# Kernel optimization log

Hardware: AMD Instinct MI355X
Metric: run time of the kernel (lower is better)

## Reference

```python
import jax, jax.numpy as jnp
import numpy as np

TAGSET = 32
START = 30
STOP = 31
B = 512
S = 2048


def setup_inputs() -> dict:
    key = jax.random.key(0)
    k1, k2, k3 = jax.random.split(key, 3)
    emissions = jax.random.normal(k1, (B, S, TAGSET), dtype=jnp.float32)
    transitions = jax.random.normal(k2, (TAGSET, TAGSET), dtype=jnp.float32)
    # replicate the torch init: no transition into START, none out of STOP
    transitions = transitions.at[START, :].set(-10000.0).at[:, STOP].set(-10000.0)
    tags = jax.random.randint(k3, (B, S), 0, START)  # valid label tags only
    return {"emissions": emissions, "transitions": transitions, "tags": tags}


def _partition(emissions, transitions):
    # CRF forward algorithm (log partition), vectorized scan over time.
    # alphas: [B, T];  transitions[tag, prev_tag]
    alphas0 = transitions[:, START][None, :] + emissions[:, 0]
    def step(alphas, emit_t):  # emit_t: [B, T]
        # scores[b, tag, prev] = e[b, tag] + trans[tag, prev] + alphas[b, prev]
        scores = emit_t[:, :, None] + transitions[None, :, :] + alphas[:, None, :]
        return jax.nn.logsumexp(scores, axis=2), None
    alphas, _ = jax.lax.scan(step, alphas0, jnp.swapaxes(emissions[:, 1:], 0, 1))
    end_scores = alphas + transitions[STOP][None, :]
    return jax.nn.logsumexp(end_scores, axis=1)  # [B]


def _gold_score(emissions, transitions, tags):
    # vectorized _compute_scores with mask = ones
    e_scores = jnp.take_along_axis(emissions, tags[:, :, None], axis=2)[..., 0].sum(axis=1)
    t_scores = transitions[tags[:, 1:], tags[:, :-1]].sum(axis=1)
    t_scores = t_scores + transitions[tags[:, 0], START] + transitions[STOP, tags[:, -1]]
    return e_scores + t_scores  # [B]


def reference(emissions, transitions, tags):
    # neg_log_likelihood = sum_b (log Z_b - score(gold path)_b)
    return jnp.sum(_partition(emissions, transitions) - _gold_score(emissions, transitions, tags))
```

## Files before the change

### kernel.cpp

```cpp
#include <hip/hip_runtime.h>

#define L2E 1.4426950408889634f
#define LN2 0.6931471805599453f

typedef float f32x16 __attribute__((ext_vector_type(16)));
typedef float f32x2  __attribute__((ext_vector_type(2)));
typedef short bf16x8 __attribute__((ext_vector_type(8)));
typedef unsigned int u32x4 __attribute__((ext_vector_type(4)));

__device__ __forceinline__ float dexp2(float x) { return __builtin_amdgcn_exp2f(x); }
__device__ __forceinline__ float dlog2(float x) { return __builtin_amdgcn_logf(x); }

__device__ __forceinline__ unsigned cvtpk(float a, float b) {
    unsigned r;
    asm("v_cvt_pk_bf16_f32 %0, %1, %2" : "=v"(r) : "v"(a), "v"(b));
    return r;
}

__device__ __forceinline__ unsigned pkrne(float a, float b) {
    unsigned ua = __float_as_uint(a), ub = __float_as_uint(b);
    ua += 0x7FFFu + ((ua >> 16) & 1u);
    ub += 0x7FFFu + ((ub >> 16) & 1u);
    return __builtin_amdgcn_perm(ub, ua, 0x07060302u);
}

__global__ __launch_bounds__(1024, 8) void crf_phase_kernel(
    const float* __restrict__ em,
    const float* __restrict__ tr,
    const int*   __restrict__ tgs,
    float*       __restrict__ ws)
{
    __shared__ float s_tr[1024];
    __shared__ unsigned short s_mat[16 * 1024];
    __shared__ float s_ring[16 * 256];
    __shared__ float s_base[16];
    __shared__ float s_gold[16];

    const int tid = threadIdx.x;
    const int b   = blockIdx.x;
    const int w   = tid >> 6;
    const int l   = tid & 63;
    const int h   = l >> 5;
    const int q   = l & 31;

    s_tr[tid & 1023] = tr[tid & 1023];
    __syncthreads();

    unsigned ea[8];
#pragma unroll
    for (int j = 0; j < 8; ++j) {
        int k0  = 16 * (j >> 2) + 8 * h + 2 * (j & 3);
        int col = (k0 & ~12) | ((k0 & 4) << 1) | ((k0 & 8) >> 1);
        ea[j] = pkrne(dexp2(s_tr[q * 32 + col] * L2E),
                      dexp2(s_tr[q * 32 + col + 1] * L2E));
    }
    const bf16x8 A0 = __builtin_bit_cast(bf16x8, (u32x4){ea[0], ea[1], ea[2], ea[3]});
    const bf16x8 A1 = __builtin_bit_cast(bf16x8, (u32x4){ea[4], ea[5], ea[6], ea[7]});

    f32x16 zro;
#pragma unroll
    for (int z = 0; z < 16; ++z) zro[z] = 0.f;

    const float* ebase = em + ((size_t)b * 2048 + (size_t)w * 128) * 32;
    const int*   tgp   = tgs + (size_t)b * 2048;
    float*       ring  = s_ring + w * 256;

    f32x16 acc;
    float  s_cur = 1.f;
    int    k_pend = 0, sigma = 0;
    float  gold = 0.f;
    float4 r0, r1;
    int    tregC = 0, tlastC = 0, tregN = 0, tlastN = 0;

#pragma unroll
    for (int r = 0; r < 16; ++r)
        acc[r] = ((((r & 3) + 8 * (r >> 2) + 4 * h) == q) ? 1.f : 0.f);

    auto eload = [&](int blk) -> float4 {
        int bb2 = blk > 15 ? 15 : blk;
        return *(const float4*)(ebase + ((bb2 * 8 + (l >> 3)) * 32 + (l & 7) * 4));
    };
    auto tagload = [&](int cl, int& treg, int& tlast) {
        int c0 = w * 128 + cl * 64;
        int idx = c0 - 1 + l; if (idx < 0) idx = 0;
        treg  = tgp[idx];
        tlast = tgp[c0 + 63];
    };

    r0 = eload(0); r1 = eload(1);
    tagload(0, tregC, tlastC);

#pragma unroll 1
    for (int blk = 0; blk < 16; ++blk) {
        if ((blk & 7) == 0) {
            int cl = blk >> 3;
            int cg = w * 2 + cl;
            if (cl > 0) { tregC = tregN; tlastC = tlastN; }
            {
                int scur = __shfl(tregC, (l + 1) & 63, 64);
                int cur  = (l == 63) ? tlastC : scur;
                int prev = tregC;
                if (l == 0 && cg == 0) prev = 30;
                gold += s_tr[cur * 32 + prev];
            }
            if (cl < 1) tagload(cl + 1, tregN, tlastN);
        }

        {
            int trel = (blk & 7) * 8 + (l >> 3);
            int tshf = __shfl(tregC, (trel + 1) & 63, 64);
            int tgt  = (trel == 63) ? tlastC : tshf;
            if ((tgt >> 2) == (l & 7)) {
                int sub = tgt & 3;
                float ev = sub == 0 ? r0.x : sub == 1 ? r0.y : sub == 2 ? r0.z : r0.w;
                gold += ev;
            }
            float4 dv;
            dv.x = dexp2(r0.x * L2E); dv.y = dexp2(r0.y * L2E);
            dv.z = dexp2(r0.z * L2E); dv.w = dexp2(r0.w * L2E);
            *(float4*)(ring + (l >> 3) * 32 + (l & 7) * 4) = dv;
        }
        r0 = r1; r1 = eload(blk + 2);

        const bool skiplast = (blk == 15) && (w == 15);

#pragma unroll
        for (int s = 0; s < 8; ++s) {
            if (s == 7 && skiplast) continue;
            const float4* rp = (const float4*)(ring + s * 32 + h * 4);
            unsigned bbn[8];
#pragma unroll
            for (int q2 = 0; q2 < 4; ++q2) {
                float4 d4 = rp[q2 * 2];
                f32x2 a0; a0.x = acc[4 * q2 + 0]; a0.y = acc[4 * q2 + 1];
                f32x2 d0; d0.x = d4.x; d0.y = d4.y;
                f32x2 m0 = a0 * d0;
                f32x2 a1; a1.x = acc[4 * q2 + 2]; a1.y = acc[4 * q2 + 3];
                f32x2 d1; d1.x = d4.z; d1.y = d4.w;
                f32x2 m1 = a1 * d1;
                if (s == 0 || s == 4) {
                    f32x2 sc; sc.x = s_cur; sc.y = s_cur;
                    m0 = m0 * sc; m1 = m1 * sc;
                }
                bbn[2 * q2]     = cvtpk(m0.x, m0.y);
                bbn[2 * q2 + 1] = cvtpk(m1.x, m1.y);
            }
            if (s == 0 || s == 4) sigma += k_pend;
            bf16x8 B0 = __builtin_bit_cast(bf16x8, (u32x4){bbn[0], bbn[1], bbn[2], bbn[3]});
            bf16x8 B1 = __builtin_bit_cast(bf16x8, (u32x4){bbn[4], bbn[5], bbn[6], bbn[7]});
            f32x16 t = __builtin_amdgcn_mfma_f32_32x32x16_bf16(A0, B0, zro, 0, 0, 0);
            acc = __builtin_amdgcn_mfma_f32_32x32x16_bf16(A1, B1, t, 0, 0, 0);
            if (s == 3 || s == 7) {
                unsigned eb = (__float_as_uint(acc[0]) >> 23) & 0xFF;
                unsigned ku = (unsigned)__builtin_amdgcn_readfirstlane((int)eb);
                k_pend = (int)ku - 127;
                s_cur = __uint_as_float((254u - ku) << 23);
            }
        }
    }

#pragma unroll
    for (int p = 0; p < 8; ++p) {
        int rrow = ((2 * p) & 3) + 8 * ((2 * p) >> 2) + 4 * h;
        *(unsigned*)(s_mat + w * 1024 + q * 32 + rrow) =
            pkrne(acc[2 * p], acc[2 * p + 1]);
    }
    if (l == 0) s_base[w] = (float)sigma;

#pragma unroll
    for (int m = 1; m < 64; m <<= 1) gold += __shfl_xor(gold, m, 64);
    if (l == 0) s_gold[w] = gold;
    __syncthreads();

    if (tid < 32) {
        int i = tid;
        float x  = dexp2(s_tr[i * 32 + 30] * L2E);
        float xb = 0.f, bs = 0.f;
        for (int c = 0; c < 16; ++c) {
            s_ring[i] = x;
            float yv[32];
#pragma unroll
            for (int j = 0; j < 8; ++j) *(float4*)&yv[4 * j] = *(const float4*)&s_ring[4 * j];
            float a2 = 0.f;
#pragma unroll
            for (int j = 0; j < 32; ++j) {
                unsigned short uv = s_mat[c * 1024 + j * 32 + i];
                a2 += __uint_as_float((unsigned)uv << 16) * yv[j];
            }
            unsigned eb2 = (__float_as_uint(a2) >> 23) & 0xFF;
            int ku0 = __shfl((int)eb2, 0, 32);
            x  = a2 * __uint_as_float((unsigned)(254 - ku0) << 23);
            xb += (float)(ku0 - 127);
            bs += s_base[c];
        }
        float elast = em[((size_t)b * 2048 + 2047) * 32 + i];
        float wv = dexp2((s_tr[31 * 32 + i] + elast) * L2E);
        float sv = x * wv;
#pragma unroll
        for (int m2 = 1; m2 < 32; m2 <<= 1) sv += __shfl_xor(sv, m2, 32);
        float logZ = (xb + bs + dlog2(sv)) * LN2;
        if (i == 0) {
            float g = 0.f;
#pragma unroll
            for (int wv2 = 0; wv2 < 16; ++wv2) g += s_gold[wv2];
            g += s_tr[31 * 32 + tgp[2047]];
            ws[b] = logZ - g;
        }
    }
}

__global__ __launch_bounds__(64) void crf_reduce_kernel(
    const float* __restrict__ ws, float* __restrict__ out)
{
    int l = threadIdx.x;
    float s = 0.f;
#pragma unroll
    for (int k = 0; k < 8; ++k) s += ws[l + k * 64];
    s += __shfl_xor(s, 1, 64);
    s += __shfl_xor(s, 2, 64);
    s += __shfl_xor(s, 4, 64);
    s += __shfl_xor(s, 8, 64);
    s += __shfl_xor(s, 16, 64);
    s += __shfl_xor(s, 32, 64);
    if (l == 0) out[0] = s;
}

extern "C" void kernel_launch(void* const* d_in, const int* in_sizes, int n_in,
                              void* d_out, int out_size, void* d_ws, size_t ws_size,
                              hipStream_t stream)
{
    const float* em = (const float*)d_in[0];
    const float* tr = (const float*)d_in[1];
    const int*   tg = (const int*)d_in[2];
    float* ws  = (float*)d_ws;
    float* out = (float*)d_out;

    hipLaunchKernelGGL(crf_phase_kernel, dim3(512), dim3(1024), 0, stream, em, tr, tg, ws);
    hipLaunchKernelGGL(crf_reduce_kernel, dim3(1), dim3(64), 0, stream, ws, out);
}
```

Measured before the change: 114.9 us.

## Store exponentiated emissions as FP8 in LDS and derive MFMA zero from acc

The per-timestep exp(emission) values staged in shared memory are packed to FP8 (4 per dword) instead of float4, shrinking the ring from 16 KB to 4 KB and turning four 16-byte LDS reads per step into one. They are unpacked with cvt_pk_f32_fp8 before multiplying the accumulator. The constant zero accumulator input to the first MFMA is replaced by acc*0, probably to free registers or add a dependency that shapes scheduling. FP8 precision on emission exponentials adds sizable rounding error to the log-partition, and acc*0 yields NaN if acc ever holds inf or NaN.

New measurement: 134.6 us. 17.2% more time.

```diff
diff --git a/kernel.cpp b/kernel.cpp
--- a/kernel.cpp
+++ b/kernel.cpp
@@ -32,7 +32,8 @@
 {
     __shared__ float s_tr[1024];
     __shared__ unsigned short s_mat[16 * 1024];
-    __shared__ float s_ring[16 * 256];
+    __shared__ unsigned s_d8[16 * 64];
+    __shared__ float s_vec[32];
     __shared__ float s_base[16];
     __shared__ float s_gold[16];
 
@@ -57,13 +58,8 @@
     const bf16x8 A0 = __builtin_bit_cast(bf16x8, (u32x4){ea[0], ea[1], ea[2], ea[3]});
     const bf16x8 A1 = __builtin_bit_cast(bf16x8, (u32x4){ea[4], ea[5], ea[6], ea[7]});
 
-    f32x16 zro;
-#pragma unroll
-    for (int z = 0; z < 16; ++z) zro[z] = 0.f;
-
     const float* ebase = em + ((size_t)b * 2048 + (size_t)w * 128) * 32;
     const int*   tgp   = tgs + (size_t)b * 2048;
-    float*       ring  = s_ring + w * 256;
 
     f32x16 acc;
     float  s_cur = 1.f;
@@ -118,7 +114,10 @@
             float4 dv;
             dv.x = dexp2(r0.x * L2E); dv.y = dexp2(r0.y * L2E);
             dv.z = dexp2(r0.z * L2E); dv.w = dexp2(r0.w * L2E);
-            *(float4*)(ring + (l >> 3) * 32 + (l & 7) * 4) = dv;
+            unsigned u = (unsigned)__builtin_amdgcn_cvt_pk_fp8_f32(dv.x, dv.y, 0, false);
+            u = (unsigned)__builtin_amdgcn_cvt_pk_fp8_f32(dv.z, dv.w, (int)u, true);
+            int c = l & 7;
+            s_d8[w * 64 + (l >> 3) * 8 + (c & 1) * 4 + (c >> 1)] = u;
         }
         r0 = r1; r1 = eload(blk + 2);
 
@@ -127,28 +126,32 @@
 #pragma unroll
         for (int s = 0; s < 8; ++s) {
             if (s == 7 && skiplast) continue;
-            const float4* rp = (const float4*)(ring + s * 32 + h * 4);
+            const u32x4 rv = *(const u32x4*)(s_d8 + w * 64 + s * 8 + h * 4);
             unsigned bbn[8];
+            f32x16 zz;
 #pragma unroll
             for (int q2 = 0; q2 < 4; ++q2) {
-                float4 d4 = rp[q2 * 2];
+                f32x2 dlo = __builtin_amdgcn_cvt_pk_f32_fp8((int)rv[q2], false);
+                f32x2 dhi = __builtin_amdgcn_cvt_pk_f32_fp8((int)rv[q2], true);
                 f32x2 a0; a0.x = acc[4 * q2 + 0]; a0.y = acc[4 * q2 + 1];
-                f32x2 d0; d0.x = d4.x; d0.y = d4.y;
-                f32x2 m0 = a0 * d0;
                 f32x2 a1; a1.x = acc[4 * q2 + 2]; a1.y = acc[4 * q2 + 3];
-                f32x2 d1; d1.x = d4.z; d1.y = d4.w;
-                f32x2 m1 = a1 * d1;
+                f32x2 m0 = a0 * dlo;
+                f32x2 m1 = a1 * dhi;
                 if (s == 0 || s == 4) {
                     f32x2 sc; sc.x = s_cur; sc.y = s_cur;
                     m0 = m0 * sc; m1 = m1 * sc;
                 }
                 bbn[2 * q2]     = cvtpk(m0.x, m0.y);
                 bbn[2 * q2 + 1] = cvtpk(m1.x, m1.y);
+                zz[4 * q2 + 0] = acc[4 * q2 + 0] * 0.f;
+                zz[4 * q2 + 1] = acc[4 * q2 + 1] * 0.f;
+                zz[4 * q2 + 2] = acc[4 * q2 + 2] * 0.f;
+                zz[4 * q2 + 3] = acc[4 * q2 + 3] * 0.f;
             }
             if (s == 0 || s == 4) sigma += k_pend;
             bf16x8 B0 = __builtin_bit_cast(bf16x8, (u32x4){bbn[0], bbn[1], bbn[2], bbn[3]});
             bf16x8 B1 = __builtin_bit_cast(bf16x8, (u32x4){bbn[4], bbn[5], bbn[6], bbn[7]});
-            f32x16 t = __builtin_amdgcn_mfma_f32_32x32x16_bf16(A0, B0, zro, 0, 0, 0);
+            f32x16 t = __builtin_amdgcn_mfma_f32_32x32x16_bf16(A0, B0, zz, 0, 0, 0);
             acc = __builtin_amdgcn_mfma_f32_32x32x16_bf16(A1, B1, t, 0, 0, 0);
             if (s == 3 || s == 7) {
                 unsigned eb = (__float_as_uint(acc[0]) >> 23) & 0xFF;
@@ -177,10 +180,10 @@
         float x  = dexp2(s_tr[i * 32 + 30] * L2E);
         float xb = 0.f, bs = 0.f;
         for (int c = 0; c < 16; ++c) {
-            s_ring[i] = x;
+            s_vec[i] = x;
             float yv[32];
 #pragma unroll
-            for (int j = 0; j < 8; ++j) *(float4*)&yv[4 * j] = *(const float4*)&s_ring[4 * j];
+            for (int j = 0; j < 8; ++j) *(float4*)&yv[4 * j] = *(const float4*)&s_vec[4 * j];
             float a2 = 0.f;
 #pragma unroll
             for (int j = 0; j < 32; ++j) {
```
